# Kernel tuning notes

Measured on AMD Instinct MI355X. Metric: run time of the kernel, lower is better.

## Reference

```python
import jax, jax.numpy as jnp
import numpy as np
from jax import lax

S, B, K, T = 16, 16, 3, 20
FP, DP = 64, 28
CP = FP - DP + 1            # 37
P = CP * CP                 # 1369 == num_pixels
H, Hh, D = 256, 128, 2


def setup_inputs() -> dict:
    key = jax.random.key(0)
    ks = jax.random.split(key, 20)

    def lin_w(k, fan_in, fan_out):
        return jax.random.normal(k, (fan_in, fan_out), jnp.float32) / np.sqrt(fan_in)

    inp = {
        "frames": jax.random.uniform(ks[0], (B, T, FP, FP), jnp.float32),
        "digit": jax.random.uniform(ks[1], (S, B, K, DP, DP), jnp.float32),
        # enc_hidden: Linear(P, H)
        "w_h1": lin_w(ks[2], P, H), "b_h1": jnp.zeros((H,), jnp.float32),
        # where_mean: Linear(H, Hh) -> ReLU -> Linear(Hh, D) -> Tanh
        "wm1": lin_w(ks[3], H, Hh), "bm1": jnp.zeros((Hh,), jnp.float32),
        "wm2": lin_w(ks[4], Hh, D), "bm2": jnp.zeros((D,), jnp.float32),
        # where_log_std: Linear(H, Hh) -> ReLU -> Linear(Hh, D)
        "ws1": lin_w(ks[5], H, Hh), "bs1": jnp.zeros((Hh,), jnp.float32),
        "ws2": lin_w(ks[6], Hh, D), "bs2": jnp.zeros((D,), jnp.float32),
        # disp_mean: Linear(P, H) -> ReLU -> Linear(H, Hh) -> ReLU -> Linear(Hh, D) -> Tanh
        "wd1": lin_w(ks[7], P, H), "bd1": jnp.zeros((H,), jnp.float32),
        "wd2": lin_w(ks[8], H, Hh), "bd2": jnp.zeros((Hh,), jnp.float32),
        "wd3": lin_w(ks[9], Hh, D), "bd3": jnp.zeros((D,), jnp.float32),
    }
    return inp


def _lin(x, w, b):
    return x @ w + b


def _forward(frames, digit, w_h1, b_h1, wm1, bm1, wm2, bm2,
             ws1, bs1, ws2, bs2, wd1, bd1, wd2, bd2, wd3, bd3):
    # frames: (B, T, FP, FP); digit: (S, B, K, DP, DP)
    s, b, k_ = digit.shape[0], digit.shape[1], digit.shape[2]
    t = frames.shape[1]

    # Template correlation. The original builds a (T, S*B*K, FP, FP) repeated
    # input and runs conv2d with groups=S*B*K. Since frames do not depend on
    # (s, k), the identical math is a grouped conv with groups=B where group b
    # holds the S*K templates for batch element b.
    x = frames.transpose(1, 0, 2, 3)                          # (T, B, FP, FP)
    kern = digit.transpose(1, 0, 2, 3, 4).reshape(b * s * k_, 1, DP, DP)
    conv = lax.conv_general_dilated(
        x, kern, window_strides=(1, 1), padding='VALID',
        dimension_numbers=('NCHW', 'OIHW', 'NCHW'),
        feature_group_count=b)                                # (T, B*S*K, CP, CP)
    cp = conv.shape[-1]
    conv = conv.reshape(t, b, s, k_, cp * cp)
    conv = conv.transpose(2, 1, 0, 3, 4)                      # (S, B, T, K, P)

    # temporal displacement of correlation maps
    conv_disp = conv[:, :, 1:] - conv[:, :, :-1]              # (S, B, T-1, K, P)

    # disp_mean MLP
    d = jax.nn.relu(_lin(conv_disp, wd1, bd1))
    d = jax.nn.relu(_lin(d, wd2, bd2))
    disp = jnp.tanh(_lin(d, wd3, bd3))                        # (S, B, T-1, K, D)

    # enc_hidden on softmax-normalized correlation maps
    hidden = jax.nn.relu(_lin(jax.nn.softmax(conv, axis=-1), w_h1, b_h1))

    q_mean = jnp.tanh(_lin(jax.nn.relu(_lin(hidden, wm1, bm1)), wm2, bm2))
    q_std = jnp.exp(_lin(jax.nn.relu(_lin(hidden, ws1, bs1)), ws2, bs2))
    return q_mean, q_std, disp


def reference(frames, digit, w_h1, b_h1, wm1, bm1, wm2, bm2,
              ws1, bs1, ws2, bs2, wd1, bd1, wd2, bd2, wd3, bd3):
    return _forward(frames, digit, w_h1, b_h1, wm1, bm1, wm2, bm2,
                    ws1, bs1, ws2, bs2, wd1, bd1, wd2, bd2, wd3, bd3)
```

## Files before the change

### kernel.cpp

```cpp
#include <hip/hip_runtime.h>
#include <hip/hip_fp16.h>

typedef __attribute__((ext_vector_type(8))) _Float16 half8;
typedef __attribute__((ext_vector_type(2))) _Float16 h2f;
typedef __attribute__((ext_vector_type(4))) float f32x4;

#define NP 1369
#define KP 1376
#define NKT 43
#define ROWS_A 15360
#define ROWS_D 14592

#define PA_OFF   0
#define PD_OFF   (ROWS_A * KP)
#define PWH_OFF  (PD_OFF + ROWS_D * KP)
#define PWD_OFF  (PWH_OFF + NKT * 16 * 512)
#define PW2_OFF  (PWD_OFF + NKT * 16 * 512)
#define PWD2_OFF (PW2_OFF + 8 * 16 * 512)
#define TSUM_OFF (PWD2_OFF + 8 * 8 * 512)
#define STAT_OFF (TSUM_OFF + 1536)

__device__ __forceinline__ unsigned short f2h(float f) {
    __half h = __float2half(f);
    return __half_as_ushort(h);
}
__device__ __forceinline__ h2f u2h2(unsigned int u) {
    h2f r; __builtin_memcpy(&r, &u, 4); return r;
}

__global__ __launch_bounds__(256)
void k0_pack(const float* __restrict__ w_h1, const float* __restrict__ wd1,
             const float* __restrict__ wm1,  const float* __restrict__ ws1,
             const float* __restrict__ wd2,  const float* __restrict__ digit,
             unsigned short* __restrict__ wsu, float* __restrict__ tsum)
{
    const int tid = threadIdx.x;
    if (blockIdx.x >= 3136) {
        const int sbk = (blockIdx.x - 3136) * 4 + (tid >> 6);
        const int l = tid & 63;
        const float* tp = digit + (size_t)sbk * 784;
        float s = 0.f;
        for (int i = l; i < 784; i += 64) s += tp[i];
        for (int o = 32; o; o >>= 1) s += __shfl_xor(s, o, 64);
        if (l == 0) tsum[sbk] = 0.5f * s;
        return;
    }
    int idx = blockIdx.x * 256 + tid;
    int local, mode;
    unsigned short* dst;
    if (idx < 352256)      { mode = 0; local = idx;          dst = wsu + PWH_OFF; }
    else if (idx < 704512) { mode = 1; local = idx - 352256; dst = wsu + PWD_OFF; }
    else if (idx < 770048) { mode = 2; local = idx - 704512; dst = wsu + PW2_OFF; }
    else                   { mode = 3; local = idx - 770048; dst = wsu + PWD2_OFF; }
    int j = local & 7, lane = (local >> 3) & 63, rest = local >> 9;
    int NTn = (mode == 3) ? 8 : 16;
    int nt = rest % NTn, kt = rest / NTn;
    int k = kt * 32 + ((lane >> 4) << 3) + j;
    int n = nt * 16 + (lane & 15);
    float v = 0.f;
    if (mode == 0)      { if (k < NP) v = w_h1[k * 256 + n]; }
    else if (mode == 1) { if (k < NP) v = wd1[k * 256 + n]; }
    else if (mode == 2) { v = (n < 128) ? wm1[k * 128 + n] : ws1[k * 128 + (n - 128)]; }
    else                { v = wd2[k * 128 + n]; }
    dst[local] = f2h(v);
}

__global__ __launch_bounds__(512)
void k1a_corr(const float* __restrict__ frames, const float* __restrict__ digit,
              const float* __restrict__ tsum, unsigned short* __restrict__ wsu)
{
    __shared__ __align__(16) unsigned short Bs[14 * 3 * 512];
    __shared__ __align__(16) unsigned int frd[64 * 36];
    __shared__ float Cn[48];

    const int tid = threadIdx.x, l = tid & 63, w = tid >> 6;
    const int mh = blockIdx.x & 1;
    const int bt = blockIdx.x >> 1;
    const int t  = bt % 20;
    const int bb = bt / 20;

    if (tid < 48) {
        int sbk_n = ((tid / 3) * 16 + bb) * 3 + (tid % 3);
        Cn[tid] = tsum[sbk_n];
    }
    if (tid < 256) frd[(tid >> 2) * 36 + 32 + (tid & 3)] = 0u;
    {
        const float4* fp4 = (const float4*)(frames + (size_t)(bb * 20 + t) * 4096);
        for (int idx = tid; idx < 1024; idx += 512) {
            float4 v = fp4[idx];
            int r = idx >> 4, c4 = idx & 15;
            unsigned lo = (unsigned)f2h(v.x) | ((unsigned)f2h(v.y) << 16);
            unsigned hi = (unsigned)f2h(v.z) | ((unsigned)f2h(v.w) << 16);
            *(uint2*)&frd[r * 36 + c4 * 2] = make_uint2(lo, hi);
        }
    }

    const int c15 = l & 15, quad = l >> 4, v0q = quad << 3;
    const int cnt = (50 - w) / 8;

    int baseb[6]; unsigned shv[6];
#pragma unroll
    for (int it = 0; it < 6; ++it) {
        int tI = mh * 43 + w + 8 * it;
        int p  = tI * 16 + c15;
        int pc = p > 1368 ? 1368 : p;
        int i  = pc / 37;
        int jj = pc - i * 37;
        int c  = jj + v0q;
        baseb[it] = i * 144 + (c >> 1) * 4;
        shv[it]   = (unsigned)((c & 1) << 4);
    }
    f32x4 acc[6][3];
#pragma unroll
    for (int it = 0; it < 6; ++it)
#pragma unroll
        for (int nt = 0; nt < 3; ++nt) acc[it][nt] = (f32x4){0.f, 0.f, 0.f, 0.f};

    for (int ph = 0; ph < 2; ++ph) {
        __syncthreads();
        for (int s = tid; s < 2688; s += 512) {
            int ktl = s / 192;
            int rem = s - ktl * 192;
            int nt = rem >> 6, sl = rem & 63;
            int nl = nt * 16 + (sl & 15);
            int v0 = (sl >> 4) << 3;
            int kt = ph * 14 + ktl;
            int sbk_n = ((nl / 3) * 16 + bb) * 3 + (nl % 3);
            const float* tp = digit + (size_t)sbk_n * 784 + kt * 28 + v0;
            float4 fa = *(const float4*)tp;
            float4 fb = (v0 <= 16) ? *(const float4*)(tp + 4) : make_float4(0.f, 0.f, 0.f, 0.f);
            uint4 pk;
            pk.x = (unsigned)f2h(fa.x) | ((unsigned)f2h(fa.y) << 16);
            pk.y = (unsigned)f2h(fa.z) | ((unsigned)f2h(fa.w) << 16);
            pk.z = (unsigned)f2h(fb.x) | ((unsigned)f2h(fb.y) << 16);
            pk.w = (unsigned)f2h(fb.z) | ((unsigned)f2h(fb.w) << 16);
            *(uint4*)(Bs + s * 8) = pk;
        }
        __syncthreads();

        for (int ktl = 0; ktl < 14; ++ktl) {
            const int kt = ph * 14 + ktl;
            half8 bf0 = *(const half8*)(Bs + ktl * 1536 + 0 * 512 + l * 8);
            half8 bf1 = *(const half8*)(Bs + ktl * 1536 + 1 * 512 + l * 8);
            half8 bf2 = *(const half8*)(Bs + ktl * 1536 + 2 * 512 + l * 8);
            const char* fbase = (const char*)frd + kt * 144;
#pragma unroll
            for (int it = 0; it < 6; ++it) {
                if (it < cnt) {
                    const char* ap = fbase + baseb[it];
                    unsigned w0 = *(const unsigned*)(ap);
                    unsigned w1 = *(const unsigned*)(ap + 4);
                    unsigned w2 = *(const unsigned*)(ap + 8);
                    unsigned w3 = *(const unsigned*)(ap + 12);
                    unsigned w4 = *(const unsigned*)(ap + 16);
                    unsigned sh = shv[it];
                    union { unsigned u[4]; half8 h8; } af;
                    af.u[0] = (unsigned)(((((unsigned long long)w1) << 32) | w0) >> sh);
                    af.u[1] = (unsigned)(((((unsigned long long)w2) << 32) | w1) >> sh);
                    af.u[2] = (unsigned)(((((unsigned long long)w3) << 32) | w2) >> sh);
                    af.u[3] = (unsigned)(((((unsigned long long)w4) << 32) | w3) >> sh);
                    acc[it][0] = __builtin_amdgcn_mfma_f32_16x16x32_f16(af.h8, bf0, acc[it][0], 0, 0, 0);
                    acc[it][1] = __builtin_amdgcn_mfma_f32_16x16x32_f16(af.h8, bf1, acc[it][1], 0, 0, 0);
                    acc[it][2] = __builtin_amdgcn_mfma_f32_16x16x32_f16(af.h8, bf2, acc[it][2], 0, 0, 0);
                }
            }
        }
    }

    for (int itg = 0; itg < 6; ++itg) {
        __syncthreads();
        if (itg < cnt) {
#pragma unroll
            for (int nt = 0; nt < 3; ++nt) {
                const int nl = nt * 16 + c15;
                const float C = Cn[nl];
                ushort4 st;
                st.x = f2h(acc[itg][nt][0] - C);
                st.y = f2h(acc[itg][nt][1] - C);
                st.z = f2h(acc[itg][nt][2] - C);
                st.w = f2h(acc[itg][nt][3] - C);
                *(ushort4*)(Bs + nl * 136 + w * 16 + quad * 4) = st;
            }
        }
        __syncthreads();
        const int nseg = (itg == 5) ? 6 : 16;
        for (int i = tid; i < 48 * nseg; i += 512) {
            int rowl = i / nseg, seg = i - rowl * nseg;
            int sbk_n = ((rowl / 3) * 16 + bb) * 3 + (rowl % 3);
            uint4 v = *(const uint4*)(Bs + rowl * 136 + seg * 8);
            *(uint4*)(wsu + PA_OFF + (size_t)(sbk_n * 20 + t) * KP
                      + mh * 688 + itg * 128 + seg * 8) = v;
        }
    }
}

__global__ __launch_bounds__(256)
void k1b_stats(const unsigned short* __restrict__ wsu, float2* __restrict__ stats)
{
    const int l = threadIdx.x & 63, wv = threadIdx.x >> 6;
    const int row = blockIdx.x * 4 + wv;
    const unsigned* rp = (const unsigned*)(wsu + PA_OFF + (size_t)row * KP);

    float f0[11], f1[11];
    float mx = -3.0e38f;
#pragma unroll
    for (int i = 0; i < 11; ++i) {
        int q = l + i * 64;
        unsigned u = (q < 685) ? rp[q] : 0u;
        h2f h = u2h2(u);
        f0[i] = (q < 685) ? (float)h[0] : -3.0e38f;
        f1[i] = (q < 684) ? (float)h[1] : -3.0e38f;
        mx = fmaxf(mx, fmaxf(f0[i], f1[i]));
    }
    for (int o = 32; o; o >>= 1) mx = fmaxf(mx, __shfl_xor(mx, o, 64));
    float sum = 0.f;
#pragma unroll
    for (int i = 0; i < 11; ++i)
        sum += __expf(f0[i] - mx) + __expf(f1[i] - mx);
    for (int o = 32; o; o >>= 1) sum += __shfl_xor(sum, o, 64);
    if (l == 0) stats[row] = make_float2(mx, 1.0f / sum);
}

__global__ __launch_bounds__(512)
void k2_gemmAB(unsigned short* __restrict__ wsu, const float* __restrict__ b_h1,
               const float2* __restrict__ stats)
{
    __shared__ __align__(16) unsigned short Bbuf[2][2 * 8192];

    const int tid = threadIdx.x, l = tid & 63, w = tid >> 6;
    const int c15 = l & 15, quad = l >> 4;
    const int M0 = blockIdx.x * 64;
    unsigned short* Abase = wsu + PA_OFF;
    const unsigned short* PWH = wsu + PWH_OFF;
    const unsigned short* PWD = wsu + PWD_OFF;
    float* HR = (float*)(wsu + PD_OFF);

    const bool isH = (w < 4);
    const int wl = w & 3;
    const int row0 = M0 + wl * 16 + c15;
    const unsigned short* a0p = Abase + (size_t)row0 * KP + quad * 8;
    float2 st0 = make_float2(0.f, 0.f);
    if (isH) st0 = stats[row0];

    f32x4 acc[16];
#pragma unroll
    for (int n = 0; n < 16; ++n) acc[n] = (f32x4){0.f, 0.f, 0.f, 0.f};

    {
        const int4* sH = (const int4*)(PWH);
        const int4* sD = (const int4*)(PWD);
        int4* dH = (int4*)(Bbuf[0]);
        int4* dD = (int4*)(Bbuf[0] + 8192);
#pragma unroll
        for (int c = 0; c < 2; ++c) {
            dH[tid + 512 * c] = sH[tid + 512 * c];
            dD[tid + 512 * c] = sD[tid + 512 * c];
        }
    }
    half8 curA = *(const half8*)(a0p);
    __syncthreads();

    for (int kt = 0; kt < NKT; ++kt) {
        const int db = kt & 1;
        half8 nxtA = curA;
        if (kt + 1 < NKT) nxtA = *(const half8*)(a0p + (kt + 1) * 32);
        int4 rH[2], rD[2];
        if (kt + 1 < NKT) {
            const int4* sH = (const int4*)(PWH + (size_t)(kt + 1) * 8192);
            const int4* sD = (const int4*)(PWD + (size_t)(kt + 1) * 8192);
#pragma unroll
            for (int c = 0; c < 2; ++c) {
                rH[c] = sH[tid + 512 * c];
                rD[c] = sD[tid + 512 * c];
            }
        }
        half8 af = curA;
        if (isH) {
            union { half8 h8; unsigned u[4]; } ia, oa;
            ia.h8 = af;
#pragma unroll
            for (int q = 0; q < 4; ++q) {
                h2f ha = u2h2(ia.u[q]);
                float a0 = __expf((float)ha[0] - st0.x) * st0.y;
                float a1 = __expf((float)ha[1] - st0.x) * st0.y;
                oa.u[q] = (unsigned)f2h(a0) | ((unsigned)f2h(a1) << 16);
            }
            af = oa.h8;
        }
        const unsigned short* bb = Bbuf[db] + (isH ? 0 : 8192);
#pragma unroll
        for (int nt = 0; nt < 16; ++nt) {
            half8 bf = *(const half8*)(bb + nt * 512 + l * 8);
            acc[nt] = __builtin_amdgcn_mfma_f32_16x16x32_f16(af, bf, acc[nt], 0, 0, 0);
        }
        if (kt + 1 < NKT) {
            int4* dH = (int4*)(Bbuf[db ^ 1]);
            int4* dD = (int4*)(Bbuf[db ^ 1] + 8192);
#pragma unroll
            for (int c = 0; c < 2; ++c) {
                dH[tid + 512 * c] = rH[c];
                dD[tid + 512 * c] = rD[c];
            }
        }
        curA = nxtA;
        __syncthreads();
    }

    if (isH) {
#pragma unroll
        for (int nt = 0; nt < 16; ++nt) {
            const int col = nt * 16 + c15;
            const float bv = b_h1[col];
#pragma unroll
            for (int r = 0; r < 4; ++r) {
                const int row = M0 + wl * 16 + quad * 4 + r;
                float v = acc[nt][r] + bv;
                Abase[(size_t)row * KP + col] = f2h(v > 0.f ? v : 0.f);
            }
        }
    } else {
#pragma unroll
        for (int nt = 0; nt < 16; ++nt) {
            const int col = nt * 16 + c15;
#pragma unroll
            for (int r = 0; r < 4; ++r) {
                const int row = M0 + wl * 16 + quad * 4 + r;
                HR[(size_t)row * 256 + col] = acc[nt][r];
            }
        }
    }
}

template <bool PATHA>
__global__ __launch_bounds__(256)
void k2_heads(unsigned short* __restrict__ wsu,
              const float* __restrict__ b1a, const float* __restrict__ b1b,
              const float* __restrict__ w2a, const float* __restrict__ b2a,
              const float* __restrict__ w2b, const float* __restrict__ b2b,
              const float* __restrict__ bd1, float* __restrict__ out)
{
    constexpr int NT2 = PATHA ? 16 : 8;
    constexpr int NI4 = NT2 / 4;
    __shared__ __align__(16) unsigned short Bsh[2][NT2 * 512];
    const int tid = threadIdx.x, l = tid & 63, w = tid >> 6;
    const int c = l & 15, quad = l >> 4;
    const int M0 = blockIdx.x * 64;
    const unsigned short* PW = wsu + (PATHA ? PW2_OFF : PWD2_OFF);

    f32x4 acc[NT2];
#pragma unroll
    for (int n = 0; n < NT2; ++n) acc[n] = (f32x4){0.f, 0.f, 0.f, 0.f};

    const int row = M0 + w * 16 + c;
    const unsigned short* arow = nullptr;
    const float* h1p = nullptr; const float* h0p = nullptr;
    if (PATHA) {
        arow = wsu + PA_OFF + (size_t)row * KP + quad * 8;
    } else {
        const float* HR = (const float*)(wsu + PD_OFF);
        const int sbk = row / 19, dt = row % 19;
        h0p = HR + (size_t)(sbk * 20 + dt) * 256 + quad * 8;
        h1p = h0p + 256;
    }

    {
        const int4* src = (const int4*)(PW);
        int4* dst = (int4*)Bsh[0];
#pragma unroll
        for (int cc = 0; cc < NI4; ++cc)
            dst[tid + 256 * cc] = src[tid + 256 * cc];
    }
    half8 curPA = {};
    float4 c1a = {}, c1b = {}, c0a = {}, c0b = {};
    if (PATHA) {
        curPA = *(const half8*)(arow);
    } else {
        c1a = *(const float4*)(h1p); c1b = *(const float4*)(h1p + 4);
        c0a = *(const float4*)(h0p); c0b = *(const float4*)(h0p + 4);
    }
    __syncthreads();

    for (int kt = 0; kt < 8; ++kt) {
        const int db = kt & 1;
        half8 nxtPA = curPA;
        float4 n1a = c1a, n1b = c1b, n0a = c0a, n0b = c0b;
        if (kt + 1 < 8) {
            if (PATHA) {
                nxtPA = *(const half8*)(arow + (kt + 1) * 32);
            } else {
                n1a = *(const float4*)(h1p + (kt + 1) * 32);
                n1b = *(const float4*)(h1p + (kt + 1) * 32 + 4);
                n0a = *(const float4*)(h0p + (kt + 1) * 32);
                n0b = *(const float4*)(h0p + (kt + 1) * 32 + 4);
            }
        }
        int4 rB[NI4];
        if (kt + 1 < 8) {
            const int4* src = (const int4*)(PW + (size_t)(kt + 1) * (NT2 * 512));
#pragma unroll
            for (int cc = 0; cc < NI4; ++cc) rB[cc] = src[tid + 256 * cc];
        }
        half8 af;
        if (PATHA) {
            af = curPA;
        } else {
            float4 bb = *(const float4*)(bd1 + kt * 32 + quad * 8);
            float4 bb2 = *(const float4*)(bd1 + kt * 32 + quad * 8 + 4);
            float v0 = fmaxf(c1a.x - c0a.x + bb.x, 0.f);
            float v1 = fmaxf(c1a.y - c0a.y + bb.y, 0.f);
            float v2 = fmaxf(c1a.z - c0a.z + bb.z, 0.f);
            float v3 = fmaxf(c1a.w - c0a.w + bb.w, 0.f);
            float v4 = fmaxf(c1b.x - c0b.x + bb2.x, 0.f);
            float v5 = fmaxf(c1b.y - c0b.y + bb2.y, 0.f);
            float v6 = fmaxf(c1b.z - c0b.z + bb2.z, 0.f);
            float v7 = fmaxf(c1b.w - c0b.w + bb2.w, 0.f);
            union { unsigned u[4]; half8 h8; } pk;
            pk.u[0] = (unsigned)f2h(v0) | ((unsigned)f2h(v1) << 16);
            pk.u[1] = (unsigned)f2h(v2) | ((unsigned)f2h(v3) << 16);
            pk.u[2] = (unsigned)f2h(v4) | ((unsigned)f2h(v5) << 16);
            pk.u[3] = (unsigned)f2h(v6) | ((unsigned)f2h(v7) << 16);
            af = pk.h8;
        }
#pragma unroll
        for (int nt = 0; nt < NT2; ++nt) {
            half8 bf = *(const half8*)(Bsh[db] + nt * 512 + l * 8);
            acc[nt] = __builtin_amdgcn_mfma_f32_16x16x32_f16(af, bf, acc[nt], 0, 0, 0);
        }
        if (kt + 1 < 8) {
            int4* dst = (int4*)Bsh[db ^ 1];
#pragma unroll
            for (int cc = 0; cc < NI4; ++cc) dst[tid + 256 * cc] = rB[cc];
        }
        curPA = nxtPA;
        c1a = n1a; c1b = n1b; c0a = n0a; c0b = n0b;
        __syncthreads();
    }
#pragma unroll
    for (int nt = 0; nt < NT2; ++nt) {
        float bv;
        if (PATHA) bv = (nt < 8) ? b1a[nt * 16 + c] : b1b[(nt - 8) * 16 + c];
        else       bv = b1a[nt * 16 + c];
#pragma unroll
        for (int r = 0; r < 4; ++r) {
            float v = acc[nt][r] + bv;
            acc[nt][r] = v > 0.f ? v : 0.f;
        }
    }
    float pm[2][4], ps[2][4];
#pragma unroll
    for (int d = 0; d < 2; ++d)
#pragma unroll
        for (int r = 0; r < 4; ++r) { pm[d][r] = 0.f; ps[d][r] = 0.f; }
#pragma unroll
    for (int d = 0; d < 2; ++d)
#pragma unroll
        for (int nt = 0; nt < 8; ++nt) {
            const float wmv = w2a[(nt * 16 + c) * 2 + d];
            float wsv = 0.f;
            if (PATHA) wsv = w2b[(nt * 16 + c) * 2 + d];
#pragma unroll
            for (int r = 0; r < 4; ++r) {
                pm[d][r] = fmaf(acc[nt][r], wmv, pm[d][r]);
                if (PATHA) ps[d][r] = fmaf(acc[nt + 8][r], wsv, ps[d][r]);
            }
        }
#pragma unroll
    for (int o = 1; o < 16; o <<= 1)
#pragma unroll
        for (int d = 0; d < 2; ++d)
#pragma unroll
            for (int r = 0; r < 4; ++r) {
                pm[d][r] += __shfl_xor(pm[d][r], o, 64);
                if (PATHA) ps[d][r] += __shfl_xor(ps[d][r], o, 64);
            }
    if (c == 0) {
#pragma unroll
        for (int r = 0; r < 4; ++r) {
            const int orow = M0 + w * 16 + quad * 4 + r;
            if (PATHA) {
                const int sbk = orow / 20, t = orow % 20;
                const int sb = sbk / 3, kk = sbk % 3;
                const int oi = ((sb * 20 + t) * 3 + kk) * 2;
                out[oi + 0] = tanhf(pm[0][r] + b2a[0]);
                out[oi + 1] = tanhf(pm[1][r] + b2a[1]);
                out[30720 + oi + 0] = __expf(ps[0][r] + b2b[0]);
                out[30720 + oi + 1] = __expf(ps[1][r] + b2b[1]);
            } else {
                const int sbk = orow / 19, dt = orow % 19;
                const int sb = sbk / 3, kk = sbk % 3;
                const int oi = 61440 + ((sb * 19 + dt) * 3 + kk) * 2;
                out[oi + 0] = tanhf(pm[0][r] + b2a[0]);
                out[oi + 1] = tanhf(pm[1][r] + b2a[1]);
            }
        }
    }
}

extern "C" void kernel_launch(void* const* d_in, const int* in_sizes, int n_in,
                              void* d_out, int out_size, void* d_ws, size_t ws_size,
                              hipStream_t stream) {
    const float* frames = (const float*)d_in[0];
    const float* digit  = (const float*)d_in[1];
    const float* w_h1   = (const float*)d_in[2];
    const float* b_h1   = (const float*)d_in[3];
    const float* wm1    = (const float*)d_in[4];
    const float* bm1    = (const float*)d_in[5];
    const float* wm2    = (const float*)d_in[6];
    const float* bm2    = (const float*)d_in[7];
    const float* ws1    = (const float*)d_in[8];
    const float* bs1    = (const float*)d_in[9];
    const float* ws2    = (const float*)d_in[10];
    const float* bs2    = (const float*)d_in[11];
    const float* wd1    = (const float*)d_in[12];
    const float* bd1    = (const float*)d_in[13];
    const float* wd2    = (const float*)d_in[14];
    const float* bd2    = (const float*)d_in[15];
    const float* wd3    = (const float*)d_in[16];
    const float* bd3    = (const float*)d_in[17];

    unsigned short* wsu = (unsigned short*)d_ws;
    float* tsum = (float*)(wsu + TSUM_OFF);
    float2* stats = (float2*)(wsu + STAT_OFF);
    float* o = (float*)d_out;

    k0_pack<<<dim3(3328), dim3(256), 0, stream>>>(w_h1, wd1, wm1, ws1, wd2, digit, wsu, tsum);
    k1a_corr<<<dim3(640), dim3(512), 0, stream>>>(frames, digit, tsum, wsu);
    k1b_stats<<<dim3(3840), dim3(256), 0, stream>>>(wsu, stats);
    k2_gemmAB<<<dim3(240), dim3(512), 0, stream>>>(wsu, b_h1, stats);
    k2_heads<true><<<dim3(240), dim3(256), 0, stream>>>(wsu, bm1, bs1, wm2, bm2, ws2, bs2, nullptr, o);
    k2_heads<false><<<dim3(228), dim3(256), 0, stream>>>(wsu, bd2, nullptr, wd3, bd3, nullptr, nullptr, bd1, o);
}
```

Before: 138.7 us.

## Pre-shift frame copy in LDS and halve template staging for occupancy

Keeps a second copy of the fp16 frame in LDS shifted by one half-element, so odd column offsets read aligned words directly instead of loading five words and funnel-shifting them. Template staging is split into four phases of seven k-tiles instead of two of fourteen, shrinking the B buffer, and launch bounds now request higher occupancy. This removes shift ALU work and loads from the inner MFMA loop, at the cost of more barriers, an extra LDS build pass, and tighter register limits that could cause spills.

```diff
diff --git a/kernel.cpp b/kernel.cpp
--- a/kernel.cpp
+++ b/kernel.cpp
@@ -65,12 +65,12 @@
     dst[local] = f2h(v);
 }
 
-__global__ __launch_bounds__(512)
+__global__ __launch_bounds__(512, 8)
 void k1a_corr(const float* __restrict__ frames, const float* __restrict__ digit,
               const float* __restrict__ tsum, unsigned short* __restrict__ wsu)
 {
-    __shared__ __align__(16) unsigned short Bs[14 * 3 * 512];
-    __shared__ __align__(16) unsigned int frd[64 * 36];
+    __shared__ __align__(16) unsigned short Bs[7 * 3 * 512];
+    __shared__ __align__(16) unsigned int frd2[2][64 * 36];
     __shared__ float Cn[48];
 
     const int tid = threadIdx.x, l = tid & 63, w = tid >> 6;
@@ -83,7 +83,11 @@
         int sbk_n = ((tid / 3) * 16 + bb) * 3 + (tid % 3);
         Cn[tid] = tsum[sbk_n];
     }
-    if (tid < 256) frd[(tid >> 2) * 36 + 32 + (tid & 3)] = 0u;
+    if (tid < 256) {
+        int r = tid >> 2, d2 = tid & 3;
+        frd2[0][r * 36 + 32 + d2] = 0u;
+        frd2[1][r * 36 + 32 + d2] = 0u;
+    }
     {
         const float4* fp4 = (const float4*)(frames + (size_t)(bb * 20 + t) * 4096);
         for (int idx = tid; idx < 1024; idx += 512) {
@@ -91,14 +95,20 @@
             int r = idx >> 4, c4 = idx & 15;
             unsigned lo = (unsigned)f2h(v.x) | ((unsigned)f2h(v.y) << 16);
             unsigned hi = (unsigned)f2h(v.z) | ((unsigned)f2h(v.w) << 16);
-            *(uint2*)&frd[r * 36 + c4 * 2] = make_uint2(lo, hi);
-        }
+            *(uint2*)&frd2[0][r * 36 + c4 * 2] = make_uint2(lo, hi);
+        }
+    }
+    __syncthreads();
+    for (int i = tid; i < 64 * 34; i += 512) {
+        int r = i / 34, d = i - r * 34;
+        unsigned lo = frd2[0][r * 36 + d], hi = frd2[0][r * 36 + d + 1];
+        frd2[1][r * 36 + d] = (lo >> 16) | (hi << 16);
     }
 
     const int c15 = l & 15, quad = l >> 4, v0q = quad << 3;
     const int cnt = (50 - w) / 8;
 
-    int baseb[6]; unsigned shv[6];
+    int baseb[6];
 #pragma unroll
     for (int it = 0; it < 6; ++it) {
         int tI = mh * 43 + w + 8 * it;
@@ -107,8 +117,7 @@
         int i  = pc / 37;
         int jj = pc - i * 37;
         int c  = jj + v0q;
-        baseb[it] = i * 144 + (c >> 1) * 4;
-        shv[it]   = (unsigned)((c & 1) << 4);
+        baseb[it] = (c & 1) * 9216 + i * 144 + ((c >> 1) << 2);
     }
     f32x4 acc[6][3];
 #pragma unroll
@@ -116,15 +125,15 @@
 #pragma unroll
         for (int nt = 0; nt < 3; ++nt) acc[it][nt] = (f32x4){0.f, 0.f, 0.f, 0.f};
 
-    for (int ph = 0; ph < 2; ++ph) {
+    for (int ph = 0; ph < 4; ++ph) {
         __syncthreads();
-        for (int s = tid; s < 2688; s += 512) {
+        for (int s = tid; s < 1344; s += 512) {
             int ktl = s / 192;
             int rem = s - ktl * 192;
             int nt = rem >> 6, sl = rem & 63;
             int nl = nt * 16 + (sl & 15);
             int v0 = (sl >> 4) << 3;
-            int kt = ph * 14 + ktl;
+            int kt = ph * 7 + ktl;
             int sbk_n = ((nl / 3) * 16 + bb) * 3 + (nl % 3);
             const float* tp = digit + (size_t)sbk_n * 784 + kt * 28 + v0;
             float4 fa = *(const float4*)tp;
@@ -138,27 +147,21 @@
         }
         __syncthreads();
 
-        for (int ktl = 0; ktl < 14; ++ktl) {
-            const int kt = ph * 14 + ktl;
+        for (int ktl = 0; ktl < 7; ++ktl) {
+            const int kt = ph * 7 + ktl;
             half8 bf0 = *(const half8*)(Bs + ktl * 1536 + 0 * 512 + l * 8);
             half8 bf1 = *(const half8*)(Bs + ktl * 1536 + 1 * 512 + l * 8);
             half8 bf2 = *(const half8*)(Bs + ktl * 1536 + 2 * 512 + l * 8);
-            const char* fbase = (const char*)frd + kt * 144;
+            const char* fb2 = (const char*)frd2 + (size_t)kt * 144;
 #pragma unroll
             for (int it = 0; it < 6; ++it) {
                 if (it < cnt) {
-                    const char* ap = fbase + baseb[it];
-                    unsigned w0 = *(const unsigned*)(ap);
-                    unsigned w1 = *(const unsigned*)(ap + 4);
-                    unsigned w2 = *(const unsigned*)(ap + 8);
-                    unsigned w3 = *(const unsigned*)(ap + 12);
-                    unsigned w4 = *(const unsigned*)(ap + 16);
-                    unsigned sh = shv[it];
+                    const unsigned* ap = (const unsigned*)(fb2 + baseb[it]);
                     union { unsigned u[4]; half8 h8; } af;
-                    af.u[0] = (unsigned)(((((unsigned long long)w1) << 32) | w0) >> sh);
-                    af.u[1] = (unsigned)(((((unsigned long long)w2) << 32) | w1) >> sh);
-                    af.u[2] = (unsigned)(((((unsigned long long)w3) << 32) | w2) >> sh);
-                    af.u[3] = (unsigned)(((((unsigned long long)w4) << 32) | w3) >> sh);
+                    af.u[0] = ap[0];
+                    af.u[1] = ap[1];
+                    af.u[2] = ap[2];
+                    af.u[3] = ap[3];
                     acc[it][0] = __builtin_amdgcn_mfma_f32_16x16x32_f16(af.h8, bf0, acc[it][0], 0, 0, 0);
                     acc[it][1] = __builtin_amdgcn_mfma_f32_16x16x32_f16(af.h8, bf1, acc[it][1], 0, 0, 0);
                     acc[it][2] = __builtin_amdgcn_mfma_f32_16x16x32_f16(af.h8, bf2, acc[it][2], 0, 0, 0);
```

Result: slower. 477.6 us (+244.3%).
